# Performance work log

Hardware: AMD Instinct MI355X
Metric: run time of the kernel (lower is better)

## Reference

```python
import jax, jax.numpy as jnp
import numpy as np

N, E, D, H = 50000, 800000, 64, 2
DH = D // H  # per-head GAT width
BN_EPS = 1e-5


def _linear_params(key, fan_in, fan_out):
    k1, k2 = jax.random.split(key)
    s = 1.0 / np.sqrt(fan_in)
    W = jax.random.uniform(k1, (fan_in, fan_out), jnp.float32, -s, s)
    b = jax.random.uniform(k2, (fan_out,), jnp.float32, -s, s)
    return W, b


def setup_inputs() -> dict:
    key = jax.random.key(0)
    ks = jax.random.split(key, 12)
    node_feats = jax.random.normal(ks[0], (N, D), jnp.float32)
    edge_feats = jax.random.normal(ks[1], (E, D), jnp.float32)
    src = jax.random.randint(ks[2], (E,), 0, N)
    dst = jax.random.randint(ks[3], (E,), 0, N)
    W_sg, b_sg = _linear_params(ks[4], D, D)
    W_dg, b_dg = _linear_params(ks[5], D, D)
    W_eg, b_eg = _linear_params(ks[6], D, D)
    W_su, b_su = _linear_params(ks[7], D, D)
    W_du, b_du = _linear_params(ks[8], D, D)
    W_gat, _ = _linear_params(ks[9], D, H * DH)
    b_gat = jnp.zeros((H * DH,), jnp.float32)
    ka, kb = jax.random.split(ks[10])
    attn_l = jax.random.normal(ka, (H, DH), jnp.float32) * 0.1
    attn_r = jax.random.normal(kb, (H, DH), jnp.float32) * 0.1
    return dict(node_feats=node_feats, edge_feats=edge_feats, src=src, dst=dst,
                W_sg=W_sg, b_sg=b_sg, W_dg=W_dg, b_dg=b_dg, W_eg=W_eg, b_eg=b_eg,
                W_su=W_su, b_su=b_su, W_du=W_du, b_du=b_du,
                W_gat=W_gat, b_gat=b_gat, attn_l=attn_l, attn_r=attn_r,
                bn_n_gamma=jnp.ones((D,), jnp.float32), bn_n_beta=jnp.zeros((D,), jnp.float32),
                bn_e_gamma=jnp.ones((D,), jnp.float32), bn_e_beta=jnp.zeros((D,), jnp.float32))


def _batchnorm(x, gamma, beta):
    # training-mode BatchNorm1d: biased variance over the batch dim
    mean = x.mean(0)
    var = x.var(0)
    return (x - mean) * jax.lax.rsqrt(var + BN_EPS) * gamma + beta


def _forward(node_feats, edge_feats, src, dst,
             W_sg, b_sg, W_dg, b_dg, W_eg, b_eg, W_su, b_su, W_du, b_du,
             W_gat, b_gat, attn_l, attn_r,
             bn_n_gamma, bn_n_beta, bn_e_gamma, bn_e_beta):
    n = node_feats.shape[0]
    # gated edge features: u_add_v + edge_gate
    e_src = node_feats @ W_sg + b_sg
    e_dst = node_feats @ W_dg + b_dg
    m = e_src[src] + e_dst[dst] + (edge_feats @ W_eg + b_eg)  # [E, D]

    # GATConv(num_heads=H) applied to src_update(node_feats)
    h = node_feats @ W_su + b_su
    feat = (h @ W_gat).reshape(n, H, DH)          # [N, H, DH]
    el = (feat * attn_l[None]).sum(-1)            # [N, H]
    er = (feat * attn_r[None]).sum(-1)            # [N, H]
    logits = jax.nn.leaky_relu(el[src] + er[dst], 0.2)  # [E, H]
    # edge softmax over incoming edges of each dst node
    lmax = jax.ops.segment_max(logits, dst, num_segments=n)
    lmax = jnp.where(jnp.isfinite(lmax), lmax, 0.0)  # zero-in-degree safety
    ex = jnp.exp(logits - lmax[dst])
    denom = jax.ops.segment_sum(ex, dst, num_segments=n)
    alpha = ex / denom[dst]                        # [E, H]
    gat_out = jax.ops.segment_sum(feat[src] * alpha[:, :, None], dst, num_segments=n)
    gat_out = (gat_out + b_gat.reshape(1, H, DH)).reshape(n, H * DH)  # flatten(1)

    # sigmoid-gated message passing: u_mul_e + sum, copy_e + sum
    sigma = jax.nn.sigmoid(m)                      # [E, D]
    Bh = node_feats @ W_du + b_du
    sum_sigma_h = jax.ops.segment_sum(Bh[src] * sigma, dst, num_segments=n)
    sum_sigma = jax.ops.segment_sum(sigma, dst, num_segments=n)
    h_agg = sum_sigma_h / (sum_sigma + 1e-6)

    x = h_agg + gat_out
    x = jax.nn.silu(_batchnorm(x, bn_n_gamma, bn_n_beta))
    y = jax.nn.silu(_batchnorm(m, bn_e_gamma, bn_e_beta))
    x = node_feats + x  # residual
    y = edge_feats + y
    return x, y


def reference(node_feats, edge_feats, src, dst,
              W_sg, b_sg, W_dg, b_dg, W_eg, b_eg, W_su, b_su, W_du, b_du,
              W_gat, b_gat, attn_l, attn_r,
              bn_n_gamma, bn_n_beta, bn_e_gamma, bn_e_beta):
    return _forward(node_feats, edge_feats, src, dst,
                    W_sg, b_sg, W_dg, b_dg, W_eg, b_eg, W_su, b_su, W_du, b_du,
                    W_gat, b_gat, attn_l, attn_r,
                    bn_n_gamma, bn_n_beta, bn_e_gamma, bn_e_beta)
```

## Files before the change

kernel.cpp:

```cpp
#include <hip/hip_runtime.h>
#include <hip/hip_bf16.h>
#include <stdint.h>

typedef __bf16 bf16;
typedef __bf16 bf16x8 __attribute__((ext_vector_type(8)));
typedef float f32x4 __attribute__((ext_vector_type(4)));

struct P22 { const void* p[22]; };
struct I22 { int n[22]; };

__device__ inline float bf2f(bf16 b) { return (float)b; }
__device__ inline float us2f(unsigned short u) {
    union { unsigned int i; float f; } x; x.i = (unsigned int)u << 16; return x.f;
}
__device__ inline unsigned short f2us(bf16 b) {
    union { bf16 b; unsigned short s; } x; x.b = b; return x.s;
}

__device__ inline float gld(const void* p, long i, int f32) {
    return f32 ? ((const float*)p)[i] : bf2f(((const bf16*)p)[i]);
}
__device__ inline bf16x8 gld8(const void* p, long i, int f32) {
    bf16x8 r;
    if (f32) {
        const float* q = (const float*)p + i;
        f32x4 a = *(const f32x4*)q, b = *(const f32x4*)(q + 4);
        #pragma unroll
        for (int j = 0; j < 4; ++j) { r[j] = (bf16)a[j]; r[4 + j] = (bf16)b[j]; }
    } else {
        r = *reinterpret_cast<const bf16x8*>((const bf16*)p + i);
    }
    return r;
}
__device__ inline void ld8f(const void* p, long i, int f32, float* o) {
    if (f32) {
        const float* q = (const float*)p + i;
        f32x4 a = *(const f32x4*)q, b = *(const f32x4*)(q + 4);
        #pragma unroll
        for (int j = 0; j < 4; ++j) { o[j] = a[j]; o[4 + j] = b[j]; }
    } else {
        bf16x8 r = *reinterpret_cast<const bf16x8*>((const bf16*)p + i);
        #pragma unroll
        for (int j = 0; j < 8; ++j) o[j] = bf2f(r[j]);
    }
}
__device__ inline float fin(float v) { return isfinite(v) ? v : 0.f; }

__global__ void k_detect(P22 in, I22 sz, int* flags) {
    int t = blockIdx.x;
    if (t == 2 || t == 3) { if (threadIdx.x == 0) flags[t] = 0; return; }
    const unsigned short* u = (const unsigned short*)in.p[t];
    int pairs = sz.n[t] >> 1; if (pairs > 256) pairs = 256;
    int lane = threadIdx.x;
    int insane = 0, evenNZ = 0, oddNZ = 0;
    for (int i = lane; i < pairs; i += 64) {
        unsigned short e = u[2 * i], o = u[2 * i + 1];
        int ee = (e >> 7) & 0xFF;
        if (e != 0) { evenNZ++; if (ee > 133 || ee < 108) insane++; }
        if (o != 0) oddNZ++;
    }
    #pragma unroll
    for (int off = 1; off < 64; off <<= 1) {
        insane += __shfl_xor(insane, off, 64);
        evenNZ += __shfl_xor(evenNZ, off, 64);
        oddNZ  += __shfl_xor(oddNZ,  off, 64);
    }
    if (lane == 0) {
        int f32 = 0;
        if (insane * 4 > pairs) f32 = 1;
        else if (evenNZ == 0 && oddNZ > 0) f32 = 1;
        flags[t] = f32;
    }
}

__global__ void __launch_bounds__(256) k_prep(P22 in, const int* F, bf16* Wcat, float* bcat) {
    __shared__ float sWsu[64 * 64];
    __shared__ float sWg[64 * 64];
    int tid = threadIdx.x;
    {
        int f1 = F[10], f2 = F[14];
        #pragma unroll 4
        for (int i = tid; i < 4096; i += 256) {
            sWsu[i] = gld(in.p[10], i, f1);
            sWg[i]  = gld(in.p[14], i, f2);
        }
    }
    __syncthreads();
    int j = tid;
    int sec = j >> 6, jc = j & 63;
    if (sec < 3) {
        int wi = sec == 0 ? 4 : (sec == 1 ? 6 : 12);
        const void* W = in.p[wi]; int fW = F[wi];
        #pragma unroll 8
        for (int k = 0; k < 64; ++k) Wcat[k * 256 + j] = (bf16)gld(W, k * 64 + jc, fW);
        bcat[j] = gld(in.p[wi + 1], jc, F[wi + 1]);
    } else {
        #pragma unroll 2
        for (int k = 0; k < 64; ++k) {
            float acc = 0.f;
            #pragma unroll 8
            for (int t = 0; t < 64; ++t) acc += sWsu[k * 64 + t] * sWg[t * 64 + jc];
            Wcat[k * 256 + j] = (bf16)acc;
        }
        float acc = gld(in.p[15], jc, F[15]);
        #pragma unroll 8
        for (int t = 0; t < 64; ++t) acc += gld(in.p[11], t, F[11]) * sWg[t * 64 + jc];
        bcat[j] = acc;
    }
}

__global__ void __launch_bounds__(256) k_node_gemm(P22 in, const int* F, const bf16* Wcat,
                                                   const float* bcat, bf16* NT2, ushort4* PG,
                                                   float* el, float* er, int N) {
    __shared__ bf16 tile[16][260];
    __shared__ float sal[64], sar[64];
    if (threadIdx.x < 64) sal[threadIdx.x] = gld(in.p[16], threadIdx.x, F[16]);
    else if (threadIdx.x < 128) sar[threadIdx.x - 64] = gld(in.p[17], threadIdx.x - 64, F[17]);

    int f0 = F[0];
    int lane = threadIdx.x & 63;
    int w = threadIdx.x >> 6;
    int col0 = w * 64, q = lane >> 4, li = lane & 15;
    bf16x8 bfr[4][2];
    #pragma unroll
    for (int t = 0; t < 4; ++t)
        #pragma unroll
        for (int h = 0; h < 2; ++h)
            #pragma unroll
            for (int j = 0; j < 8; ++j)
                bfr[t][h][j] = Wcat[(long)(h * 32 + q * 8 + j) * 256 + col0 + t * 16 + li];
    float bias[4];
    #pragma unroll
    for (int t = 0; t < 4; ++t) bias[t] = bcat[col0 + t * 16 + li];

    int prow = threadIdx.x >> 4;
    int pk   = threadIdx.x & 15;
    int pc4  = pk * 4;
    int phead = pc4 >> 5;

    int ntiles = (N + 15) >> 4;
    for (int rt = blockIdx.x; rt < ntiles; rt += gridDim.x) {
        int row0 = rt * 16;
        int rload = min(row0 + li, N - 1);
        bf16x8 a0 = gld8(in.p[0], (long)rload * 64 + (q << 3), f0);
        bf16x8 a1 = gld8(in.p[0], (long)rload * 64 + 32 + (q << 3), f0);
        #pragma unroll
        for (int t = 0; t < 4; ++t) {
            f32x4 acc = {0.f, 0.f, 0.f, 0.f};
            acc = __builtin_amdgcn_mfma_f32_16x16x32_bf16(a0, bfr[t][0], acc, 0, 0, 0);
            acc = __builtin_amdgcn_mfma_f32_16x16x32_bf16(a1, bfr[t][1], acc, 0, 0, 0);
            int col = col0 + t * 16 + li;
            #pragma unroll
            for (int r = 0; r < 4; ++r) {
                int rr = q * 4 + r;
                bf16 bv = (bf16)(acc[r] + bias[t]);
                tile[rr][col] = bv;
                if (w < 2 && row0 + rr < N) NT2[(long)(row0 + rr) * 128 + col] = bv;
            }
        }
        __syncthreads();
        int grow = row0 + prow;
        if (grow < N) {
            #pragma unroll
            for (int j = 0; j < 4; ++j) {
                int c = pc4 + j;
                ushort4 pv;
                pv.x = f2us(tile[prow][c]);
                pv.y = f2us(tile[prow][64 + c]);
                pv.z = f2us(tile[prow][128 + c]);
                pv.w = f2us(tile[prow][192 + c]);
                PG[(long)grow * 64 + c] = pv;
            }
        }
        float pl = 0.f, pr = 0.f;
        #pragma unroll
        for (int j = 0; j < 4; ++j) {
            float f = bf2f(tile[prow][192 + pc4 + j]);
            pl += f * sal[pc4 + j];
            pr += f * sar[pc4 + j];
        }
        pl += __shfl_xor(pl, 1, 64); pr += __shfl_xor(pr, 1, 64);
        pl += __shfl_xor(pl, 2, 64); pr += __shfl_xor(pr, 2, 64);
        pl += __shfl_xor(pl, 4, 64); pr += __shfl_xor(pr, 4, 64);
        if ((pk & 7) == 0 && grow < N) {
            el[(long)grow * 2 + phead] = pl;
            er[(long)grow * 2 + phead] = pr;
        }
        __syncthreads();
    }
}

__global__ void __launch_bounds__(256) k_edge_gemm(P22 in, const int* F, bf16* Meg,
                                                   int* deg, int E) {
    int f_ef = F[1];
    int lane = threadIdx.x & 63;
    int w = threadIdx.x >> 6;
    int q = lane >> 4, li = lane & 15;
    const int* dstp = (const int*)in.p[3];
    bf16x8 bfrag[4][2];
    #pragma unroll
    for (int t = 0; t < 4; ++t)
        #pragma unroll
        for (int h = 0; h < 2; ++h)
            #pragma unroll
            for (int j = 0; j < 8; ++j)
                bfrag[t][h][j] = (bf16)gld(in.p[8], (long)(h * 32 + q * 8 + j) * 64 + t * 16 + li, F[8]);
    float bias[4];
    #pragma unroll
    for (int t = 0; t < 4; ++t) bias[t] = gld(in.p[9], t * 16 + li, F[9]);

    int ntiles = E >> 4;
    for (int et = blockIdx.x * 4 + w; et < ntiles; et += gridDim.x * 4) {
        int e0 = et * 16;
        bf16x8 a0 = gld8(in.p[1], (long)(e0 + li) * 64 + (q << 3), f_ef);
        bf16x8 a1 = gld8(in.p[1], (long)(e0 + li) * 64 + 32 + (q << 3), f_ef);
        if (lane < 16) atomicAdd(&deg[dstp[e0 + lane]], 1);
        #pragma unroll
        for (int t = 0; t < 4; ++t) {
            f32x4 c = {0.f, 0.f, 0.f, 0.f};
            c = __builtin_amdgcn_mfma_f32_16x16x32_bf16(a0, bfrag[t][0], c, 0, 0, 0);
            c = __builtin_amdgcn_mfma_f32_16x16x32_bf16(a1, bfrag[t][1], c, 0, 0, 0);
            #pragma unroll
            for (int r = 0; r < 4; ++r) {
                int row = e0 + q * 4 + r;
                Meg[(long)row * 64 + t * 16 + li] = (bf16)(c[r] + bias[t]);
            }
        }
    }
}

__global__ void __launch_bounds__(1024) k_scan(const int* deg, int* rowptr, int* cursor, int N) {
    __shared__ int sums[1024];
    int t = threadIdx.x;
    int chunk = (N + 1023) >> 10;
    int lo = t * chunk, hi = min(lo + chunk, N);
    int s = 0;
    for (int i = lo; i < hi; ++i) s += deg[i];
    int val = s;
    sums[t] = val;
    __syncthreads();
    for (int off = 1; off < 1024; off <<= 1) {
        int add = (t >= off) ? sums[t - off] : 0;
        __syncthreads();
        val += add; sums[t] = val;
        __syncthreads();
    }
    int run = val - s;
    for (int i = lo; i < hi; ++i) {
        rowptr[i] = run; cursor[i] = run;
        run += deg[i];
    }
    if (t == 1023) rowptr[N] = run;
}

__global__ void k_scatter(const int* src, const int* dst, int* cursor, int2* ES, int E) {
    for (int e = blockIdx.x * blockDim.x + threadIdx.x; e < E; e += gridDim.x * blockDim.x) {
        int pos = atomicAdd(&cursor[dst[e]], 1);
        int2 v; v.x = e; v.y = src[e];
        ES[pos] = v;
    }
}

__global__ void __launch_bounds__(256) k_agg(
    P22 in, const int* F, const ushort4* PG, const bf16* Meg,
    const float* el, const float* er, const int* rowptr, const int2* ES,
    float* v, float* bn_e_acc, float* bn_n_acc, int N) {
    int lane = threadIdx.x & 63;
    int w = threadIdx.x >> 6;
    int c = lane, h = c >> 5;
    float bg = gld(in.p[15], c, F[15]);
    float es_ = 0.f, eq = 0.f;
    float vs = 0.f, vq = 0.f;

    for (int n = blockIdx.x * 4 + w; n < N; n += gridDim.x * 4) {
        float dn = us2f(PG[(long)n * 64 + c].y);
        float errh = er[(long)n * 2 + h];
        int lo = rowptr[n], hi = rowptr[n + 1];
        float ss = 0.f, ssh = 0.f, num = 0.f, den = 0.f;
        #pragma unroll 4
        for (int j = lo; j < hi; ++j) {
            int2 e2 = ES[j];
            ushort4 g = PG[(long)e2.y * 64 + c];
            float mg = bf2f(Meg[(long)e2.x * 64 + c]);
            float srv = us2f(g.x), bh = us2f(g.z), ft = us2f(g.w);
            float mv = mg + srv + dn;
            float sg = 1.f / (1.f + __expf(-mv));
            ss += sg; ssh += bh * sg;
            es_ += mv; eq += mv * mv;
            float lg = el[(long)e2.y * 2 + h] + errh;
            lg = lg > 0.f ? lg : 0.2f * lg;
            lg = fminf(fmaxf(lg, -30.f), 30.f);
            float ex = __expf(lg);
            den += ex; num += ft * ex;
        }
        float hagg = ssh / (ss + 1e-6f);
        float gat = den > 0.f ? num / den : 0.f;
        float vv = hagg + gat + bg;
        v[(long)n * 64 + c] = vv;
        vs += vv; vq += vv * vv;
    }

    __shared__ float r1[256], r2[256];
    r1[threadIdx.x] = es_; r2[threadIdx.x] = eq;
    __syncthreads();
    if (threadIdx.x < 64) {
        atomicAdd(bn_e_acc + c,      r1[c] + r1[64 + c] + r1[128 + c] + r1[192 + c]);
        atomicAdd(bn_e_acc + 64 + c, r2[c] + r2[64 + c] + r2[128 + c] + r2[192 + c]);
    }
    __syncthreads();
    r1[threadIdx.x] = vs; r2[threadIdx.x] = vq;
    __syncthreads();
    if (threadIdx.x < 64) {
        atomicAdd(bn_n_acc + c,      r1[c] + r1[64 + c] + r1[128 + c] + r1[192 + c]);
        atomicAdd(bn_n_acc + 64 + c, r2[c] + r2[64 + c] + r2[128 + c] + r2[192 + c]);
    }
}

__global__ void k_x_out(P22 in, const int* F, const float* v, const float* acc,
                        void* d_out, int N) {
    int f_out = F[0];
    int c = threadIdx.x & 63;
    int slot = threadIdx.x >> 6;
    float inv = 1.f / (float)N;
    float mean = acc[c] * inv;
    float var = fmaxf(acc[64 + c] * inv - mean * mean, 0.f);
    float rstd = rsqrtf(var + 1e-5f);
    float ga = gld(in.p[18], c, F[18]), be = gld(in.p[19], c, F[19]);
    for (int n = blockIdx.x * 4 + slot; n < N; n += gridDim.x * 4) {
        float t = (v[(long)n * 64 + c] - mean) * rstd * ga + be;
        float sl = t / (1.f + __expf(-t));
        float x = fin(gld(in.p[0], (long)n * 64 + c, F[0]) + sl);
        if (f_out) ((float*)d_out)[(long)n * 64 + c] = x;
        else       ((bf16*)d_out)[(long)n * 64 + c] = (bf16)x;
    }
}

__global__ void __launch_bounds__(256) k_edge_y(
    P22 in, const int* F, const bf16* NT2, const bf16* Meg,
    const float* bn_e_acc, void* d_out, int N, int E) {
    int f_ef = F[1], f_out = F[0];
    const int* srcp = (const int*)in.p[2];
    const int* dstp = (const int*)in.p[3];
    int tid = blockIdx.x * 256 + threadIdx.x;
    int oc = tid & 7, c0 = oc * 8;
    float mean[8], rstd[8], ga[8], be[8];
    float invE = 1.f / (float)E;
    #pragma unroll
    for (int j = 0; j < 8; ++j) {
        int c = c0 + j;
        float mn = bn_e_acc[c] * invE;
        float vr = fmaxf(bn_e_acc[64 + c] * invE - mn * mn, 0.f);
        mean[j] = mn; rstd[j] = rsqrtf(vr + 1e-5f);
        ga[j] = gld(in.p[20], c, F[20]); be[j] = gld(in.p[21], c, F[21]);
    }
    char* yb = (char*)d_out + (size_t)N * 64 * (f_out ? 4 : 2);
    int estride = (gridDim.x * 256) >> 3;
    for (long e = tid >> 3; e < E; e += estride) {
        int si = srcp[e], di = dstp[e];
        bf16x8 mg = *reinterpret_cast<const bf16x8*>(Meg + e * 64 + c0);
        bf16x8 sr = *reinterpret_cast<const bf16x8*>(NT2 + (long)si * 128 + c0);
        bf16x8 dr = *reinterpret_cast<const bf16x8*>(NT2 + (long)di * 128 + 64 + c0);
        float ef[8]; ld8f(in.p[1], e * 64 + c0, f_ef, ef);
        float y[8];
        #pragma unroll
        for (int j = 0; j < 8; ++j) {
            float mv = bf2f(mg[j]) + bf2f(sr[j]) + bf2f(dr[j]);
            float t = (mv - mean[j]) * rstd[j] * ga[j] + be[j];
            float sl = t / (1.f + __expf(-t));
            y[j] = fin(ef[j] + sl);
        }
        if (f_out) {
            float* yp = (float*)yb + e * 64 + c0;
            f32x4 y0 = {y[0], y[1], y[2], y[3]}, y1 = {y[4], y[5], y[6], y[7]};
            *(f32x4*)yp = y0; *(f32x4*)(yp + 4) = y1;
        } else {
            bf16x8 yv;
            #pragma unroll
            for (int j = 0; j < 8; ++j) yv[j] = (bf16)y[j];
            *reinterpret_cast<bf16x8*>((bf16*)yb + e * 64 + c0) = yv;
        }
    }
}

extern "C" void kernel_launch(void* const* d_in, const int* in_sizes, int n_in,
                              void* d_out, int out_size, void* d_ws, size_t ws_size,
                              hipStream_t stream) {
    P22 p; I22 sz;
    for (int i = 0; i < 22; ++i) { p.p[i] = d_in[i]; sz.n[i] = in_sizes[i]; }
    const int N = in_sizes[0] / 64;
    const int E = in_sizes[2];

    char* ws = (char*)d_ws;
    size_t off = 0;
    auto alloc = [&](size_t bytes) -> void* {
        void* ptr = ws + off;
        off = (off + bytes + 255) & ~(size_t)255;
        return ptr;
    };
    int*   flags  = (int*)    alloc(22 * 4);
    bf16*  NT2    = (bf16*)   alloc((size_t)N * 128 * 2);
    ushort4* PG   = (ushort4*)alloc((size_t)N * 64 * 8);
    float* el     = (float*)  alloc((size_t)N * 2 * 4);
    float* er     = (float*)  alloc((size_t)N * 2 * 4);
    bf16*  Wcat   = (bf16*)   alloc(64 * 256 * 2);
    float* bcat   = (float*)  alloc(256 * 4);
    bf16*  Meg    = (bf16*)   alloc((size_t)E * 64 * 2);
    int*   rowptr = (int*)    alloc((size_t)(N + 1) * 4);
    int*   cursor = (int*)    alloc((size_t)N * 4);
    int2*  ES     = (int2*)   alloc((size_t)E * 8);
    float* v      = (float*)  alloc((size_t)N * 64 * 4);
    char* zbase = ws + off;
    int*   deg      = (int*)  alloc((size_t)N * 4);
    float* bn_e_acc = (float*)alloc(128 * 4);
    float* bn_n_acc = (float*)alloc(128 * 4);
    size_t zbytes = (size_t)((ws + off) - zbase);
    hipMemsetAsync(zbase, 0, zbytes, stream);

    const int* srcp = (const int*)d_in[2];
    const int* dstp = (const int*)d_in[3];

    hipLaunchKernelGGL(k_detect, dim3(22), dim3(64), 0, stream, p, sz, flags);
    hipLaunchKernelGGL(k_prep, dim3(1), dim3(256), 0, stream, p, flags, Wcat, bcat);
    hipLaunchKernelGGL(k_node_gemm, dim3(800), dim3(256), 0, stream,
                       p, flags, Wcat, bcat, NT2, PG, el, er, N);
    hipLaunchKernelGGL(k_edge_gemm, dim3(1024), dim3(256), 0, stream, p, flags, Meg, deg, E);
    hipLaunchKernelGGL(k_scan, dim3(1), dim3(1024), 0, stream, deg, rowptr, cursor, N);
    hipLaunchKernelGGL(k_scatter, dim3(1024), dim3(256), 0, stream, srcp, dstp, cursor, ES, E);
    hipLaunchKernelGGL(k_agg, dim3(2048), dim3(256), 0, stream,
                       p, flags, PG, Meg, el, er, rowptr, ES, v, bn_e_acc, bn_n_acc, N);
    hipLaunchKernelGGL(k_x_out, dim3(512), dim3(256), 0, stream, p, flags, v, bn_n_acc, d_out, N);
    hipLaunchKernelGGL(k_edge_y, dim3(2048), dim3(256), 0, stream,
                       p, flags, NT2, Meg, bn_e_acc, d_out, N, E);
}
```

Measured before the change: 919.1 us.

## Fold node gathers into edge GEMM to materialize full edge messages once

The edge GEMM kernel now gathers the src and dst node projections itself, adds them to the edge linear output, stores the complete message m, and accumulates the edge BatchNorm sums there. Downstream aggregation and edge-output kernels read m directly instead of regathering e_src/e_dst, and the per-node pack shrinks from four to two bf16 channels. This removes two random row gathers per edge in the final edge pass and a gather in aggregation, and cuts the width of the packed per-node buffer. In exchange the edge GEMM does scalar, uncoalesced per-element gathers (16 per lane per tile), which may be less efficient than the vectorized gathers they replace.

```diff
diff --git a/kernel.cpp b/kernel.cpp
--- a/kernel.cpp
+++ b/kernel.cpp
@@ -110,8 +110,8 @@
 }
 
 __global__ void __launch_bounds__(256) k_node_gemm(P22 in, const int* F, const bf16* Wcat,
-                                                   const float* bcat, bf16* NT2, ushort4* PG,
-                                                   float* el, float* er, int N) {
+                                                   const float* bcat, bf16* ESRC, bf16* EDST,
+                                                   ushort2* PG2, float* el, float* er, int N) {
     __shared__ bf16 tile[16][260];
     __shared__ float sal[64], sar[64];
     if (threadIdx.x < 64) sal[threadIdx.x] = gld(in.p[16], threadIdx.x, F[16]);
@@ -155,7 +155,11 @@
                 int rr = q * 4 + r;
                 bf16 bv = (bf16)(acc[r] + bias[t]);
                 tile[rr][col] = bv;
-                if (w < 2 && row0 + rr < N) NT2[(long)(row0 + rr) * 128 + col] = bv;
+                int row = row0 + rr;
+                if (row < N) {
+                    if (w == 0)      ESRC[(long)row * 64 + col] = bv;
+                    else if (w == 1) EDST[(long)row * 64 + (col - 64)] = bv;
+                }
             }
         }
         __syncthreads();
@@ -164,12 +168,10 @@
             #pragma unroll
             for (int j = 0; j < 4; ++j) {
                 int c = pc4 + j;
-                ushort4 pv;
-                pv.x = f2us(tile[prow][c]);
-                pv.y = f2us(tile[prow][64 + c]);
-                pv.z = f2us(tile[prow][128 + c]);
-                pv.w = f2us(tile[prow][192 + c]);
-                PG[(long)grow * 64 + c] = pv;
+                ushort2 pv;
+                pv.x = f2us(tile[prow][128 + c]);
+                pv.y = f2us(tile[prow][192 + c]);
+                PG2[(long)grow * 64 + c] = pv;
             }
         }
         float pl = 0.f, pr = 0.f;
@@ -190,12 +192,14 @@
     }
 }
 
-__global__ void __launch_bounds__(256) k_edge_gemm(P22 in, const int* F, bf16* Meg,
-                                                   int* deg, int E) {
+__global__ void __launch_bounds__(256) k_edge_gemm(
+    P22 in, const int* F, const bf16* ESRC, const bf16* EDST,
+    bf16* M, int* deg, float* bn_e_acc, int E) {
     int f_ef = F[1];
     int lane = threadIdx.x & 63;
     int w = threadIdx.x >> 6;
     int q = lane >> 4, li = lane & 15;
+    const int* srcp = (const int*)in.p[2];
     const int* dstp = (const int*)in.p[3];
     bf16x8 bfrag[4][2];
     #pragma unroll
@@ -208,6 +212,8 @@
     float bias[4];
     #pragma unroll
     for (int t = 0; t < 4; ++t) bias[t] = gld(in.p[9], t * 16 + li, F[9]);
+
+    float es[4] = {0.f, 0.f, 0.f, 0.f}, eq[4] = {0.f, 0.f, 0.f, 0.f};
 
     int ntiles = E >> 4;
     for (int et = blockIdx.x * 4 + w; et < ntiles; et += gridDim.x * 4) {
@@ -215,17 +221,54 @@
         bf16x8 a0 = gld8(in.p[1], (long)(e0 + li) * 64 + (q << 3), f_ef);
         bf16x8 a1 = gld8(in.p[1], (long)(e0 + li) * 64 + 32 + (q << 3), f_ef);
         if (lane < 16) atomicAdd(&deg[dstp[e0 + lane]], 1);
+        int si[4], di[4];
+        #pragma unroll
+        for (int r = 0; r < 4; ++r) {
+            int row = e0 + q * 4 + r;
+            si[r] = srcp[row]; di[r] = dstp[row];
+        }
+        bf16 sv[4][4], dv[4][4];
+        #pragma unroll
+        for (int r = 0; r < 4; ++r)
+            #pragma unroll
+            for (int t = 0; t < 4; ++t) {
+                sv[r][t] = ESRC[(long)si[r] * 64 + t * 16 + li];
+                dv[r][t] = EDST[(long)di[r] * 64 + t * 16 + li];
+            }
+        f32x4 acc[4];
         #pragma unroll
         for (int t = 0; t < 4; ++t) {
             f32x4 c = {0.f, 0.f, 0.f, 0.f};
             c = __builtin_amdgcn_mfma_f32_16x16x32_bf16(a0, bfrag[t][0], c, 0, 0, 0);
             c = __builtin_amdgcn_mfma_f32_16x16x32_bf16(a1, bfrag[t][1], c, 0, 0, 0);
-            #pragma unroll
-            for (int r = 0; r < 4; ++r) {
-                int row = e0 + q * 4 + r;
-                Meg[(long)row * 64 + t * 16 + li] = (bf16)(c[r] + bias[t]);
+            acc[t] = c;
+        }
+        #pragma unroll
+        for (int r = 0; r < 4; ++r) {
+            int row = e0 + q * 4 + r;
+            #pragma unroll
+            for (int t = 0; t < 4; ++t) {
+                float mval = acc[t][r] + bias[t] + bf2f(sv[r][t]) + bf2f(dv[r][t]);
+                M[(long)row * 64 + t * 16 + li] = (bf16)mval;
+                es[t] += mval; eq[t] += mval * mval;
             }
         }
+    }
+    __shared__ float red_s[256], red_q[256];
+    #pragma unroll
+    for (int t = 0; t < 4; ++t) {
+        float s = es[t], qq = eq[t];
+        s += __shfl_xor(s, 16, 64); s += __shfl_xor(s, 32, 64);
+        qq += __shfl_xor(qq, 16, 64); qq += __shfl_xor(qq, 32, 64);
+        if (q == 0) { red_s[w * 64 + t * 16 + li] = s; red_q[w * 64 + t * 16 + li] = qq; }
+    }
+    __syncthreads();
+    if (threadIdx.x < 64) {
+        int c = threadIdx.x;
+        float s  = red_s[c] + red_s[64 + c] + red_s[128 + c] + red_s[192 + c];
+        float qq = red_q[c] + red_q[64 + c] + red_q[128 + c] + red_q[192 + c];
+        atomicAdd(bn_e_acc + c, s);
+        atomicAdd(bn_e_acc + 64 + c, qq);
     }
 }
 
@@ -262,36 +305,31 @@
 }
 
 __global__ void __launch_bounds__(256) k_agg(
-    P22 in, const int* F, const ushort4* PG, const bf16* Meg,
+    P22 in, const int* F, const ushort2* PG2, const bf16* M,
     const float* el, const float* er, const int* rowptr, const int2* ES,
-    float* v, float* bn_e_acc, float* bn_n_acc, int N) {
+    float* v, float* bn_n_acc, int N) {
     int lane = threadIdx.x & 63;
     int w = threadIdx.x >> 6;
     int c = lane, h = c >> 5;
     float bg = gld(in.p[15], c, F[15]);
-    float es_ = 0.f, eq = 0.f;
     float vs = 0.f, vq = 0.f;
 
     for (int n = blockIdx.x * 4 + w; n < N; n += gridDim.x * 4) {
-        float dn = us2f(PG[(long)n * 64 + c].y);
         float errh = er[(long)n * 2 + h];
         int lo = rowptr[n], hi = rowptr[n + 1];
         float ss = 0.f, ssh = 0.f, num = 0.f, den = 0.f;
         #pragma unroll 4
         for (int j = lo; j < hi; ++j) {
             int2 e2 = ES[j];
-            ushort4 g = PG[(long)e2.y * 64 + c];
-            float mg = bf2f(Meg[(long)e2.x * 64 + c]);
-            float srv = us2f(g.x), bh = us2f(g.z), ft = us2f(g.w);
-            float mv = mg + srv + dn;
+            ushort2 g = PG2[(long)e2.y * 64 + c];
+            float mv = bf2f(M[(long)e2.x * 64 + c]);
             float sg = 1.f / (1.f + __expf(-mv));
-            ss += sg; ssh += bh * sg;
-            es_ += mv; eq += mv * mv;
+            ss += sg; ssh += us2f(g.x) * sg;
             float lg = el[(long)e2.y * 2 + h] + errh;
             lg = lg > 0.f ? lg : 0.2f * lg;
             lg = fminf(fmaxf(lg, -30.f), 30.f);
             float ex = __expf(lg);
-            den += ex; num += ft * ex;
+            den += ex; num += us2f(g.y) * ex;
         }
         float hagg = ssh / (ss + 1e-6f);
         float gat = den > 0.f ? num / den : 0.f;
@@ -301,13 +339,6 @@
     }
 
     __shared__ float r1[256], r2[256];
-    r1[threadIdx.x] = es_; r2[threadIdx.x] = eq;
-    __syncthreads();
-    if (threadIdx.x < 64) {
-        atomicAdd(bn_e_acc + c,      r1[c] + r1[64 + c] + r1[128 + c] + r1[192 + c]);
-        atomicAdd(bn_e_acc + 64 + c, r2[c] + r2[64 + c] + r2[128 + c] + r2[192 + c]);
-    }
-    __syncthreads();
     r1[threadIdx.x] = vs; r2[threadIdx.x] = vq;
     __syncthreads();
     if (threadIdx.x < 64) {
@@ -336,11 +367,9 @@
 }
 
 __global__ void __launch_bounds__(256) k_edge_y(
-    P22 in, const int* F, const bf16* NT2, const bf16* Meg,
-    const float* bn_e_acc, void* d_out, int N, int E) {
+    P22 in, const int* F, const bf16* M, const float* bn_e_acc,
+    void* d_out, int N, int E) {
     int f_ef = F[1], f_out = F[0];
-    const int* srcp = (const int*)in.p[2];
-    const int* dstp = (const int*)in.p[3];
     int tid = blockIdx.x * 256 + threadIdx.x;
     int oc = tid & 7, c0 = oc * 8;
     float mean[8], rstd[8], ga[8], be[8];
@@ -356,15 +385,12 @@
     char* yb = (char*)d_out + (size_t)N * 64 * (f_out ? 4 : 2);
     int estride = (gridDim.x * 256) >> 3;
     for (long e = tid >> 3; e < E; e += estride) {
-        int si = srcp[e], di = dstp[e];
-        bf16x8 mg = *reinterpret_cast<const bf16x8*>(Meg + e * 64 + c0);
-        bf16x8 sr = *reinterpret_cast<const bf16x8*>(NT2 + (long)si * 128 + c0);
-        bf16x8 dr = *reinterpret_cast<const bf16x8*>(NT2 + (long)di * 128 + 64 + c0);
+        bf16x8 mg = *reinterpret_cast<const bf16x8*>(M + e * 64 + c0);
         float ef[8]; ld8f(in.p[1], e * 64 + c0, f_ef, ef);
         float y[8];
         #pragma unroll
         for (int j = 0; j < 8; ++j) {
-            float mv = bf2f(mg[j]) + bf2f(sr[j]) + bf2f(dr[j]);
+            float mv = bf2f(mg[j]);
             float t = (mv - mean[j]) * rstd[j] * ga[j] + be[j];
             float sl = t / (1.f + __expf(-t));
             y[j] = fin(ef[j] + sl);
@@ -398,13 +424,14 @@
         return ptr;
     };
     int*   flags  = (int*)    alloc(22 * 4);
-    bf16*  NT2    = (bf16*)   alloc((size_t)N * 128 * 2);
-    ushort4* PG   = (ushort4*)alloc((size_t)N * 64 * 8);
+    bf16*  ESRC   = (bf16*)   alloc((size_t)N * 64 * 2);
+    bf16*  EDST   = (bf16*)   alloc((size_t)N * 64 * 2);
+    ushort2* PG2  = (ushort2*)alloc((size_t)N * 64 * 4);
     float* el     = (float*)  alloc((size_t)N * 2 * 4);
     float* er     = (float*)  alloc((size_t)N * 2 * 4);
     bf16*  Wcat   = (bf16*)   alloc(64 * 256 * 2);
     float* bcat   = (float*)  alloc(256 * 4);
-    bf16*  Meg    = (bf16*)   alloc((size_t)E * 64 * 2);
+    bf16*  M      = (bf16*)   alloc((size_t)E * 64 * 2);
     int*   rowptr = (int*)    alloc((size_t)(N + 1) * 4);
     int*   cursor = (int*)    alloc((size_t)N * 4);
     int2*  ES     = (int2*)   alloc((size_t)E * 8);
@@ -422,13 +449,14 @@
     hipLaunchKernelGGL(k_detect, dim3(22), dim3(64), 0, stream, p, sz, flags);
     hipLaunchKernelGGL(k_prep, dim3(1), dim3(256), 0, stream, p, flags, Wcat, bcat);
     hipLaunchKernelGGL(k_node_gemm, dim3(800), dim3(256), 0, stream,
-                       p, flags, Wcat, bcat, NT2, PG, el, er, N);
-    hipLaunchKernelGGL(k_edge_gemm, dim3(1024), dim3(256), 0, stream, p, flags, Meg, deg, E);
+                       p, flags, Wcat, bcat, ESRC, EDST, PG2, el, er, N);
+    hipLaunchKernelGGL(k_edge_gemm, dim3(1024), dim3(256), 0, stream,
+                       p, flags, ESRC, EDST, M, deg, bn_e_acc, E);
     hipLaunchKernelGGL(k_scan, dim3(1), dim3(1024), 0, stream, deg, rowptr, cursor, N);
     hipLaunchKernelGGL(k_scatter, dim3(1024), dim3(256), 0, stream, srcp, dstp, cursor, ES, E);
     hipLaunchKernelGGL(k_agg, dim3(2048), dim3(256), 0, stream,
-                       p, flags, PG, Meg, el, er, rowptr, ES, v, bn_e_acc, bn_n_acc, N);
+                       p, flags, PG2, M, el, er, rowptr, ES, v, bn_n_acc, N);
     hipLaunchKernelGGL(k_x_out, dim3(512), dim3(256), 0, stream, p, flags, v, bn_n_acc, d_out, N);
     hipLaunchKernelGGL(k_edge_y, dim3(2048), dim3(256), 0, stream,
-                       p, flags, NT2, Meg, bn_e_acc, d_out, N, E);
-}
+                       p, flags, M, bn_e_acc, d_out, N, E);
+}
```

Result: faster. 896.5 us (-2.5%).
